# Optimization experiments

Hardware: AMD Instinct MI355X
Metric: run time of the kernel (lower is better)

The kernel has to match this reference:

```python
import jax, jax.numpy as jnp
import numpy as np

B, N, D = 8, 4096, 6          # clouds, points per cloud, coordinate dim
K = 64                        # max_num_neighbors in radius query
NS1, NS2 = 2048, 512          # fps ratios 0.5 and 0.25
R1, R2 = 0.2, 0.4             # ball-query radii
DIMS = {1: [6, 64, 64, 128], 2: [134, 128, 128, 256], 3: [262, 256, 512, 1024], 4: [1024, 512, 512]}


def setup_inputs():
    key = jax.random.key(0)
    k0, k1, k2 = jax.random.split(key, 3)
    inp = {}
    inp['synapse_cordi'] = jax.random.normal(k0, (B * N, D), jnp.float32)
    inp['batch_index'] = jnp.repeat(jnp.arange(B, dtype=jnp.int32), N)
    inp['weight'] = jax.random.uniform(k1, (B * N,), jnp.float32)
    k = k2
    for i, dims in DIMS.items():
        for j in range(len(dims) - 1):
            k, kw = jax.random.split(k)
            inp[f'w{i}_{j}'] = jax.random.normal(kw, (dims[j], dims[j + 1]), jnp.float32) * (1.0 / float(np.sqrt(dims[j])))
            inp[f'b{i}_{j}'] = jnp.zeros((dims[j + 1],), jnp.float32)
    return inp


def _mlp(x, params):
    # PyG MLP, plain_last=True; batch-norm at default (eval, running stats) is identity
    n = len(params)
    for i, (W, b) in enumerate(params):
        x = x @ W + b
        if i < n - 1:
            x = jax.nn.relu(x)
    return x


def _fps(pos, n_s):
    # farthest point sampling on one cloud [N, D] -> [n_s] indices (deterministic start at 0)
    d0 = jnp.sum((pos - pos[0]) ** 2, axis=-1)
    def step(mind, _):
        nxt = jnp.argmax(mind)
        mind = jnp.minimum(mind, jnp.sum((pos - pos[nxt]) ** 2, axis=-1))
        return mind, nxt
    _, idxs = jax.lax.scan(step, d0, None, length=n_s - 1)
    return jnp.concatenate([jnp.zeros((1,), idxs.dtype), idxs])


def _ball(pos, pos_q, r):
    # radius query: up to K nearest points within r for each query; [n_q,K] idx + validity mask
    d2 = jnp.sum((pos_q[:, None, :] - pos[None, :, :]) ** 2, axis=-1)  # [n_q, N]
    neg = jnp.where(d2 <= r * r, -d2, -jnp.inf)
    vals, nbr = jax.lax.top_k(neg, K)
    return nbr, vals > -jnp.inf


def _sa(x, pos, params, n_s, r):
    # Weight_Sample_Module: fps -> radius -> PointNetConv (gather, MLP, masked max-scatter)
    idx = jax.vmap(lambda p: _fps(p, n_s))(pos)                     # [B, n_s]
    pos_q = jnp.take_along_axis(pos, idx[..., None], axis=1)        # [B, n_s, D]
    nbr, valid = jax.vmap(lambda p, q: _ball(p, q, r))(pos, pos_q)  # [B, n_s, K]
    gather = lambda a: jax.vmap(lambda t, i: t[i])(a, nbr)          # [B, n_s, K, C]
    rel = gather(pos) - pos_q[:, :, None, :]
    feat = rel if x is None else jnp.concatenate([gather(x), rel], axis=-1)
    h = _mlp(feat, params)                                          # [B, n_s, K, C_out]
    h = jnp.where(valid[..., None], h, -jnp.inf)
    return jnp.max(h, axis=2), pos_q                                # max aggregation


def reference(synapse_cordi, batch_index, weight,
              w1_0, b1_0, w1_1, b1_1, w1_2, b1_2,
              w2_0, b2_0, w2_1, b2_1, w2_2, b2_2,
              w3_0, b3_0, w3_1, b3_1, w3_2, b3_2,
              w4_0, b4_0, w4_1, b4_1):
    pos = synapse_cordi.reshape(B, N, D)  # uniform clouds; batch_index = repeat(arange(B), N)
    p1 = [(w1_0, b1_0), (w1_1, b1_1), (w1_2, b1_2)]
    p2 = [(w2_0, b2_0), (w2_1, b2_1), (w2_2, b2_2)]
    p3 = [(w3_0, b3_0), (w3_1, b3_1), (w3_2, b3_2)]
    p4 = [(w4_0, b4_0), (w4_1, b4_1)]
    x1, pos1 = _sa(None, pos, p1, NS1, R1)   # [B, 2048, 128]
    x2, pos2 = _sa(x1, pos1, p2, NS2, R2)    # [B, 512, 256]
    h = _mlp(jnp.concatenate([x2, pos2], axis=-1), p3)  # [B, 512, 1024]
    g = jnp.max(h, axis=1)                   # global max pool -> [B, 1024]
    return _mlp(g, p4)                       # [B, 512]
```

## Files before the change

### kernel.cpp

```cpp
#include <hip/hip_runtime.h>
#include <math.h>

#define B_ 8
#define N_ 4096
#define D_ 6
#define K_ 64
#define NS1_ 2048
#define NS2_ 512

typedef float v2f __attribute__((ext_vector_type(2)));


__device__ __forceinline__ float dist2_rn(const float* __restrict__ a, const float* __restrict__ q) {
    float s = 0.f;
#pragma unroll
    for (int d = 0; d < 6; ++d) {
        float diff = __fsub_rn(a[d], q[d]);
        s = __fadd_rn(s, __fmul_rn(diff, diff));
    }
    return s;
}

__device__ __forceinline__ unsigned mapf(float x) {
    unsigned u = __float_as_uint(x);
    return (u & 0x80000000u) ? ~u : (u | 0x80000000u);
}
__device__ __forceinline__ float unmapf(unsigned u) {
    return __uint_as_float((u & 0x80000000u) ? (u & 0x7FFFFFFFu) : ~u);
}

template <int CTRL>
__device__ __forceinline__ double dppd(double k) {
    int lo = __double2loint(k), hi = __double2hiint(k);
    int nlo = __builtin_amdgcn_update_dpp(lo, lo, CTRL, 0xF, 0xF, false);
    int nhi = __builtin_amdgcn_update_dpp(hi, hi, CTRL, 0xF, 0xF, false);
    return __hiloint2double(nhi, nlo);
}


__device__ __forceinline__ void wait_flag(unsigned* f, int t) {
    if (t == 0) {
        while (__hip_atomic_load(f, __ATOMIC_RELAXED, __HIP_MEMORY_SCOPE_AGENT) == 0u)
            __builtin_amdgcn_s_sleep(32);
        __builtin_amdgcn_fence(__ATOMIC_ACQUIRE, "agent");
    }
    __syncthreads();
}


template <int NP, int NS>
__device__ __forceinline__ void fps_core(float* __restrict__ spos, int* __restrict__ sidx,
                                         double* __restrict__ part, int t) {
#pragma clang fp contract(off)
    constexpr int NT = 256;
    constexpr int P = NP / NT;
    constexpr int HP = P / 2;
    int lane = t & 63, w = t >> 6;

    v2f px2[HP][6];
#pragma unroll
    for (int j = 0; j < HP; ++j)
#pragma unroll
        for (int d = 0; d < 6; ++d) {
            px2[j][d].x = spos[(t + NT * (2 * j)) * 6 + d];
            px2[j][d].y = spos[(t + NT * (2 * j + 1)) * 6 + d];
        }

    float cx[6];
#pragma unroll
    for (int d = 0; d < 6; ++d) cx[d] = spos[d];

    v2f mind2[HP];
    float runv = -1.f;
    int runj = 0;
#pragma unroll
    for (int j = 0; j < HP; ++j) {
        v2f d2 = {0.f, 0.f};
#pragma unroll
        for (int d = 0; d < 6; ++d) {
            v2f df = px2[j][d] - cx[d];
            d2 = d2 + df * df;
        }
        mind2[j] = d2;
        if (d2.x > runv) { runv = d2.x; runj = t + NT * (2 * j); }
        if (d2.y > runv) { runv = d2.y; runj = t + NT * (2 * j + 1); }
    }

    for (int s = 1; s < NS; ++s) {
        double key = __hiloint2double((int)__float_as_uint(runv), (int)(unsigned)(~runj));
        key = fmax(key, dppd<0x111>(key));
        key = fmax(key, dppd<0x112>(key));
        key = fmax(key, dppd<0x114>(key));
        key = fmax(key, dppd<0x118>(key));
        key = fmax(key, dppd<0x142>(key));
        key = fmax(key, dppd<0x143>(key));
        if (lane == 63) part[(s & 1) * 4 + w] = key;
        __syncthreads();
        double kk = part[(s & 1) * 4 + (lane & 3)];
        kk = fmax(kk, dppd<0x111>(kk));
        kk = fmax(kk, dppd<0x112>(kk));
        int nx = ~__builtin_amdgcn_readlane(__double2loint(kk), 3);
        if (t == 0) sidx[s] = nx;

        const float2* sv2 = (const float2*)spos;
        float2 ca = sv2[nx * 3], cb = sv2[nx * 3 + 1], cc = sv2[nx * 3 + 2];
        cx[0] = ca.x; cx[1] = ca.y; cx[2] = cb.x; cx[3] = cb.y; cx[4] = cc.x; cx[5] = cc.y;

        runv = -1.f;
        runj = 0;
#pragma unroll
        for (int j = 0; j < HP; ++j) {
            v2f d2 = {0.f, 0.f};
#pragma unroll
            for (int d = 0; d < 6; ++d) {
                v2f df = px2[j][d] - cx[d];
                d2 = d2 + df * df;
            }
            float mx = fminf(mind2[j].x, d2.x);
            float my = fminf(mind2[j].y, d2.y);
            mind2[j].x = mx;
            mind2[j].y = my;
            if (mx > runv) { runv = mx; runj = t + NT * (2 * j); }
            if (my > runv) { runv = my; runj = t + NT * (2 * j + 1); }
        }
    }
}


template <int NPTS, int S>
__device__ __forceinline__ int ball_scan(const float* __restrict__ sp,
                                         const float* __restrict__ posq,
                                         float r2, int qid, int tid,
                                         float* __restrict__ sd, unsigned short* __restrict__ si) {
    float q[6];
#pragma unroll
    for (int d = 0; d < 6; ++d) q[d] = posq[(size_t)qid * 6 + d];

    int n = 0;
    float thr = INFINITY;
#pragma unroll 4
    for (int j = 0; j < NPTS; ++j) {
        float d2 = dist2_rn(sp + j * 6, q);
        if (d2 <= r2 && (n < K_ || d2 < thr)) {
            int i = (n < K_) ? n : (K_ - 1);
            if (n < K_) ++n;
            while (i > 0 && sd[(i - 1) * S + tid] > d2) {
                sd[i * S + tid] = sd[(i - 1) * S + tid];
                si[i * S + tid] = si[(i - 1) * S + tid];
                --i;
            }
            sd[i * S + tid] = d2;
            si[i * S + tid] = (unsigned short)j;
            if (n == K_) thr = sd[(K_ - 1) * S + tid];
        }
    }
    return n;
}


__global__ __launch_bounds__(256, 1) void stage12_kernel(
        const float* __restrict__ pos, float* __restrict__ pos1, float* __restrict__ pos2,
        float* __restrict__ x1, int* __restrict__ nbr2, int* __restrict__ cnt2,
        unsigned* __restrict__ g, unsigned* flags,
        const float* __restrict__ W1_0, const float* __restrict__ B1_0,
        const float* __restrict__ W1_1, const float* __restrict__ B1_1,
        const float* __restrict__ W1_2, const float* __restrict__ B1_2,
        float r2_1, float r2_2) {
    __shared__ union Smem {
        struct { float spos[N_ * 6]; int sidx[NS1_]; double part[8]; } fps;
        struct { float spos[N_ * 6]; float sd[K_ * 128]; unsigned short si[K_ * 128];
                 unsigned short scnt[128]; } p1;
        struct { float spos1[NS1_ * 6]; float sd2[K_ * 64]; unsigned short si2[K_ * 64]; } b2;
    } sm;
    int t = threadIdx.x;
    int lane = t & 63, w = t >> 6;

    if (blockIdx.x < 8) {
        int b = blockIdx.x;
        float* spos = sm.fps.spos;
        int* sidx = sm.fps.sidx;
        double* part = sm.fps.part;

        {
            const float4* src = (const float4*)(pos + (size_t)b * N_ * 6);
            float4* dst = (float4*)spos;
            for (int e = t; e < N_ * 6 / 4; e += 256) dst[e] = src[e];
        }
        if (t == 0) sidx[0] = 0;
        __syncthreads();

        fps_core<N_, NS1_>(spos, sidx, part, t);
        __syncthreads();

        float smp[NS1_ / 256][6];
#pragma unroll
        for (int i = 0; i < NS1_ / 256; ++i) {
            int s = t + 256 * i;
            int ix = sidx[s];
#pragma unroll
            for (int d = 0; d < 6; ++d) smp[i][d] = spos[ix * 6 + d];
        }
#pragma unroll
        for (int i = 0; i < NS1_ / 256; ++i) {
            int s = t + 256 * i;
#pragma unroll
            for (int d = 0; d < 6; ++d) pos1[((size_t)b * NS1_ + s) * 6 + d] = smp[i][d];
        }
        __syncthreads();
        if (t == 0) {
            __threadfence();
            __hip_atomic_store(&flags[b], 1u, __ATOMIC_RELEASE, __HIP_MEMORY_SCOPE_AGENT);
        }

#pragma unroll
        for (int i = 0; i < NS1_ / 256; ++i) {
            int s = t + 256 * i;
#pragma unroll
            for (int d = 0; d < 6; ++d) spos[s * 6 + d] = smp[i][d];
        }
        for (int e = t; e < 1024; e += 256) g[b * 1024 + e] = 0u;
        if (t == 0) sidx[0] = 0;
        __syncthreads();

        fps_core<NS1_, NS2_>(spos, sidx, part, t);
        __syncthreads();

        for (int s = t; s < NS2_; s += 256) {
            int ix = sidx[s];
#pragma unroll
            for (int d = 0; d < 6; ++d) pos2[((size_t)b * NS2_ + s) * 6 + d] = spos[ix * 6 + d];
        }
        __syncthreads();
        if (t == 0) {
            __threadfence();
            __hip_atomic_store(&flags[8 + b], 1u, __ATOMIC_RELEASE, __HIP_MEMORY_SCOPE_AGENT);
        }
    } else if (blockIdx.x < 8 + 128) {
        int blk = blockIdx.x - 8;
        int b = blk >> 4;
        {
            const float4* src = (const float4*)(pos + (size_t)b * N_ * 6);
            float4* dst = (float4*)sm.p1.spos;
            for (int e = t; e < N_ * 6 / 4; e += 256) dst[e] = src[e];
        }
        __syncthreads();
        wait_flag(&flags[b], t);

        int qbase1 = b * NS1_ + (blk & 15) * 128;
        if (t < 128) {
            int n = ball_scan<N_, 128>(sm.p1.spos, pos1, r2_1, qbase1 + t, t, sm.p1.sd, sm.p1.si);
            sm.p1.scnt[t] = (unsigned short)n;
        }
        __syncthreads();

        for (int qq = 0; qq < 32; ++qq) {
            int lq = w * 32 + qq;
            int qid = qbase1 + lq;
            float q[6];
#pragma unroll
            for (int d = 0; d < 6; ++d) q[d] = pos1[(size_t)qid * 6 + d];
            int c = sm.p1.scnt[lq];
            float m0 = -INFINITY, m1 = -INFINITY;
            for (int n = 0; n < c; ++n) {
                int j = sm.p1.si[n * 128 + lq];
                float rel[6];
#pragma unroll
                for (int d = 0; d < 6; ++d) rel[d] = sm.p1.spos[j * 6 + d] - q[d];
                float a = B1_0[lane];
#pragma unroll
                for (int d = 0; d < 6; ++d) a = fmaf(W1_0[d * 64 + lane], rel[d], a);
                float h1 = fmaxf(a, 0.f);
                float a2 = B1_1[lane];
                for (int k = 0; k < 64; ++k) {
                    float v = __shfl(h1, k, 64);
                    a2 = fmaf(W1_1[k * 64 + lane], v, a2);
                }
                float h2 = fmaxf(a2, 0.f);
                float o0 = B1_2[lane], o1 = B1_2[64 + lane];
                for (int k = 0; k < 64; ++k) {
                    float v = __shfl(h2, k, 64);
                    o0 = fmaf(W1_2[k * 128 + lane], v, o0);
                    o1 = fmaf(W1_2[k * 128 + 64 + lane], v, o1);
                }
                m0 = fmaxf(m0, o0);
                m1 = fmaxf(m1, o1);
            }
            x1[(size_t)qid * 128 + lane] = m0;
            x1[(size_t)qid * 128 + 64 + lane] = m1;
        }
    } else {
        int blk = blockIdx.x - 136;
        int b = blk >> 3;
        wait_flag(&flags[b], t);
        {
            const float4* src = (const float4*)(pos1 + (size_t)b * NS1_ * 6);
            float4* dst = (float4*)sm.b2.spos1;
            for (int e = t; e < NS1_ * 6 / 4; e += 256) dst[e] = src[e];
        }
        __syncthreads();
        wait_flag(&flags[8 + b], t);
        if (t < 64) {
            int qid = blk * 64 + t;
            int n = ball_scan<NS1_, 64>(sm.b2.spos1, pos2, r2_2, qid, t, sm.b2.sd2, sm.b2.si2);
            cnt2[qid] = n;
            for (int i = 0; i < n; ++i) nbr2[(size_t)qid * K_ + i] = (int)sm.b2.si2[i * 64 + t];
        }
    }
}


__global__ __launch_bounds__(256, 1) void sa2_mlp3_kernel(
        const float* __restrict__ pos1, const float* __restrict__ pos2,
        const int* __restrict__ nbr, const int* __restrict__ cnt,
        const float* __restrict__ x1,
        const float* __restrict__ W1, const float* __restrict__ B1,
        const float* __restrict__ W2, const float* __restrict__ B2,
        const float* __restrict__ W3, const float* __restrict__ B3,
        const float* __restrict__ M0, const float* __restrict__ MB0,
        const float* __restrict__ M1, const float* __restrict__ MB1,
        const float* __restrict__ M2, const float* __restrict__ MB2,
        unsigned* __restrict__ g) {
    __shared__ float sx2[16 * 256];
    int lane = threadIdx.x & 63;
    int w = threadIdx.x >> 6;
    int qbase = blockIdx.x * 16;
    int b = qbase >> 9;

    for (int qq = 0; qq < 4; ++qq) {
        int lq = w * 4 + qq;
        int qid = qbase + lq;
        float q[6];
#pragma unroll
        for (int d = 0; d < 6; ++d) q[d] = pos2[(size_t)qid * 6 + d];
        int c = cnt[qid];
        float m0 = -INFINITY, m1 = -INFINITY, m2 = -INFINITY, m3 = -INFINITY;
        for (int n = 0; n < c; ++n) {
            int j = nbr[(size_t)qid * K_ + n];
            size_t row = (size_t)b * NS1_ + j;
            const float* xs = x1 + row * 128;
            float rel[6];
#pragma unroll
            for (int d = 0; d < 6; ++d) rel[d] = pos1[row * 6 + d] - q[d];
            float a0e = B1[lane], a0o = 0.f, a1e = B1[64 + lane], a1o = 0.f;
            for (int k = 0; k < 128; k += 2) {
                float v0 = xs[k], v1 = xs[k + 1];
                a0e = fmaf(W1[k * 128 + lane], v0, a0e);
                a1e = fmaf(W1[k * 128 + 64 + lane], v0, a1e);
                a0o = fmaf(W1[(k + 1) * 128 + lane], v1, a0o);
                a1o = fmaf(W1[(k + 1) * 128 + 64 + lane], v1, a1o);
            }
            float a0 = a0e + a0o, a1 = a1e + a1o;
#pragma unroll
            for (int d = 0; d < 6; ++d) {
                float v = rel[d];
                a0 = fmaf(W1[(128 + d) * 128 + lane], v, a0);
                a1 = fmaf(W1[(128 + d) * 128 + 64 + lane], v, a1);
            }
            float h1a = fmaxf(a0, 0.f), h1b = fmaxf(a1, 0.f);
            float c0 = B2[lane], c1 = B2[64 + lane];
            for (int k = 0; k < 64; ++k) {
                float v = __shfl(h1a, k, 64);
                c0 = fmaf(W2[k * 128 + lane], v, c0);
                c1 = fmaf(W2[k * 128 + 64 + lane], v, c1);
            }
            for (int k = 0; k < 64; ++k) {
                float v = __shfl(h1b, k, 64);
                c0 = fmaf(W2[(64 + k) * 128 + lane], v, c0);
                c1 = fmaf(W2[(64 + k) * 128 + 64 + lane], v, c1);
            }
            float h2a = fmaxf(c0, 0.f), h2b = fmaxf(c1, 0.f);
            float e0 = B3[lane], e1 = B3[64 + lane], e2 = B3[128 + lane], e3 = B3[192 + lane];
            for (int k = 0; k < 64; ++k) {
                float v = __shfl(h2a, k, 64);
                e0 = fmaf(W3[k * 256 + lane], v, e0);
                e1 = fmaf(W3[k * 256 + 64 + lane], v, e1);
                e2 = fmaf(W3[k * 256 + 128 + lane], v, e2);
                e3 = fmaf(W3[k * 256 + 192 + lane], v, e3);
            }
            for (int k = 0; k < 64; ++k) {
                float v = __shfl(h2b, k, 64);
                e0 = fmaf(W3[(64 + k) * 256 + lane], v, e0);
                e1 = fmaf(W3[(64 + k) * 256 + 64 + lane], v, e1);
                e2 = fmaf(W3[(64 + k) * 256 + 128 + lane], v, e2);
                e3 = fmaf(W3[(64 + k) * 256 + 192 + lane], v, e3);
            }
            m0 = fmaxf(m0, e0);
            m1 = fmaxf(m1, e1);
            m2 = fmaxf(m2, e2);
            m3 = fmaxf(m3, e3);
        }
        sx2[lq * 256 + lane] = m0;
        sx2[lq * 256 + 64 + lane] = m1;
        sx2[lq * 256 + 128 + lane] = m2;
        sx2[lq * 256 + 192 + lane] = m3;
    }
    __syncthreads();

    int lq0 = w * 4;
    int qid0 = qbase + lq0;

    float xr[4][4];
#pragma unroll
    for (int q = 0; q < 4; ++q)
#pragma unroll
        for (int j = 0; j < 4; ++j) xr[q][j] = sx2[(lq0 + q) * 256 + j * 64 + lane];

    float a[4][4];
    {
        float4 bv = *(const float4*)&MB0[lane * 4];
#pragma unroll
        for (int q = 0; q < 4; ++q) { a[q][0] = bv.x; a[q][1] = bv.y; a[q][2] = bv.z; a[q][3] = bv.w; }
    }
#pragma unroll
    for (int j = 0; j < 4; ++j) {
        for (int k2 = 0; k2 < 64; ++k2) {
            int k = j * 64 + k2;
            float4 wv = *(const float4*)&M0[(size_t)k * 256 + lane * 4];
#pragma unroll
            for (int q = 0; q < 4; ++q) {
                float v = __shfl(xr[q][j], k2, 64);
                a[q][0] = fmaf(wv.x, v, a[q][0]);
                a[q][1] = fmaf(wv.y, v, a[q][1]);
                a[q][2] = fmaf(wv.z, v, a[q][2]);
                a[q][3] = fmaf(wv.w, v, a[q][3]);
            }
        }
    }
#pragma unroll
    for (int d = 0; d < 6; ++d) {
        float4 wv = *(const float4*)&M0[(size_t)(256 + d) * 256 + lane * 4];
#pragma unroll
        for (int q = 0; q < 4; ++q) {
            float v = pos2[(size_t)(qid0 + q) * 6 + d];
            a[q][0] = fmaf(wv.x, v, a[q][0]);
            a[q][1] = fmaf(wv.y, v, a[q][1]);
            a[q][2] = fmaf(wv.z, v, a[q][2]);
            a[q][3] = fmaf(wv.w, v, a[q][3]);
        }
    }
    float h1[4][4];
#pragma unroll
    for (int q = 0; q < 4; ++q)
#pragma unroll
        for (int u = 0; u < 4; ++u) h1[q][u] = fmaxf(a[q][u], 0.f);

    float c[4][8];
    {
        float4 b0 = *(const float4*)&MB1[lane * 8];
        float4 b1 = *(const float4*)&MB1[lane * 8 + 4];
#pragma unroll
        for (int q = 0; q < 4; ++q) {
            c[q][0] = b0.x; c[q][1] = b0.y; c[q][2] = b0.z; c[q][3] = b0.w;
            c[q][4] = b1.x; c[q][5] = b1.y; c[q][6] = b1.z; c[q][7] = b1.w;
        }
    }
    for (int l = 0; l < 64; ++l) {
#pragma unroll
        for (int r = 0; r < 4; ++r) {
            int k = l * 4 + r;
            float4 w0 = *(const float4*)&M1[(size_t)k * 512 + lane * 8];
            float4 w1 = *(const float4*)&M1[(size_t)k * 512 + lane * 8 + 4];
#pragma unroll
            for (int q = 0; q < 4; ++q) {
                float v = __shfl(h1[q][r], l, 64);
                c[q][0] = fmaf(w0.x, v, c[q][0]);
                c[q][1] = fmaf(w0.y, v, c[q][1]);
                c[q][2] = fmaf(w0.z, v, c[q][2]);
                c[q][3] = fmaf(w0.w, v, c[q][3]);
                c[q][4] = fmaf(w1.x, v, c[q][4]);
                c[q][5] = fmaf(w1.y, v, c[q][5]);
                c[q][6] = fmaf(w1.z, v, c[q][6]);
                c[q][7] = fmaf(w1.w, v, c[q][7]);
            }
        }
    }
    float h2[4][8];
#pragma unroll
    for (int q = 0; q < 4; ++q)
#pragma unroll
        for (int u = 0; u < 8; ++u) h2[q][u] = fmaxf(c[q][u], 0.f);

    float e[4][16];
#pragma unroll
    for (int jj = 0; jj < 4; ++jj) {
        float4 bv = *(const float4*)&MB2[lane * 16 + jj * 4];
#pragma unroll
        for (int q = 0; q < 4; ++q) {
            e[q][jj * 4 + 0] = bv.x; e[q][jj * 4 + 1] = bv.y;
            e[q][jj * 4 + 2] = bv.z; e[q][jj * 4 + 3] = bv.w;
        }
    }
    for (int l = 0; l < 64; ++l) {
#pragma unroll
        for (int r = 0; r < 8; ++r) {
            int k = l * 8 + r;
            const float* wp = &M2[(size_t)k * 1024 + lane * 16];
            float4 w0 = *(const float4*)&wp[0];
            float4 w1 = *(const float4*)&wp[4];
            float4 w2 = *(const float4*)&wp[8];
            float4 w3 = *(const float4*)&wp[12];
#pragma unroll
            for (int q = 0; q < 4; ++q) {
                float v = __shfl(h2[q][r], l, 64);
                e[q][0]  = fmaf(w0.x, v, e[q][0]);
                e[q][1]  = fmaf(w0.y, v, e[q][1]);
                e[q][2]  = fmaf(w0.z, v, e[q][2]);
                e[q][3]  = fmaf(w0.w, v, e[q][3]);
                e[q][4]  = fmaf(w1.x, v, e[q][4]);
                e[q][5]  = fmaf(w1.y, v, e[q][5]);
                e[q][6]  = fmaf(w1.z, v, e[q][6]);
                e[q][7]  = fmaf(w1.w, v, e[q][7]);
                e[q][8]  = fmaf(w2.x, v, e[q][8]);
                e[q][9]  = fmaf(w2.y, v, e[q][9]);
                e[q][10] = fmaf(w2.z, v, e[q][10]);
                e[q][11] = fmaf(w2.w, v, e[q][11]);
                e[q][12] = fmaf(w3.x, v, e[q][12]);
                e[q][13] = fmaf(w3.y, v, e[q][13]);
                e[q][14] = fmaf(w3.z, v, e[q][14]);
                e[q][15] = fmaf(w3.w, v, e[q][15]);
            }
        }
    }
#pragma unroll
    for (int u = 0; u < 16; ++u) {
        float m = fmaxf(fmaxf(e[0][u], e[1][u]), fmaxf(e[2][u], e[3][u]));
        atomicMax(&g[b * 1024 + lane * 16 + u], mapf(m));
    }
}


__global__ __launch_bounds__(512) void mlp4_kernel(const unsigned* __restrict__ g,
                                                   const float* __restrict__ W0, const float* __restrict__ B0,
                                                   const float* __restrict__ W1, const float* __restrict__ B1,
                                                   float* __restrict__ out) {
    int b = blockIdx.x;
    int c = threadIdx.x;
    __shared__ float h[512];
    float a0 = B0[c], a1 = 0.f, a2 = 0.f, a3 = 0.f;
    for (int k = 0; k < 1024; k += 4) {
        float v0 = unmapf(g[b * 1024 + k]);
        float v1 = unmapf(g[b * 1024 + k + 1]);
        float v2 = unmapf(g[b * 1024 + k + 2]);
        float v3 = unmapf(g[b * 1024 + k + 3]);
        a0 = fmaf(v0, W0[k * 512 + c], a0);
        a1 = fmaf(v1, W0[(k + 1) * 512 + c], a1);
        a2 = fmaf(v2, W0[(k + 2) * 512 + c], a2);
        a3 = fmaf(v3, W0[(k + 3) * 512 + c], a3);
    }
    h[c] = fmaxf((a0 + a1) + (a2 + a3), 0.f);
    __syncthreads();
    float o0 = B1[c], o1 = 0.f, o2 = 0.f, o3 = 0.f;
    for (int k = 0; k < 512; k += 4) {
        o0 = fmaf(h[k], W1[k * 512 + c], o0);
        o1 = fmaf(h[k + 1], W1[(k + 1) * 512 + c], o1);
        o2 = fmaf(h[k + 2], W1[(k + 2) * 512 + c], o2);
        o3 = fmaf(h[k + 3], W1[(k + 3) * 512 + c], o3);
    }
    out[(size_t)b * 512 + c] = (o0 + o1) + (o2 + o3);
}


extern "C" void kernel_launch(void* const* d_in, const int* in_sizes, int n_in,
                              void* d_out, int out_size, void* d_ws, size_t ws_size,
                              hipStream_t stream) {
    const float* pos = (const float*)d_in[0];
    const float* w1_0 = (const float*)d_in[3];
    const float* b1_0 = (const float*)d_in[4];
    const float* w1_1 = (const float*)d_in[5];
    const float* b1_1 = (const float*)d_in[6];
    const float* w1_2 = (const float*)d_in[7];
    const float* b1_2 = (const float*)d_in[8];
    const float* w2_0 = (const float*)d_in[9];
    const float* b2_0 = (const float*)d_in[10];
    const float* w2_1 = (const float*)d_in[11];
    const float* b2_1 = (const float*)d_in[12];
    const float* w2_2 = (const float*)d_in[13];
    const float* b2_2 = (const float*)d_in[14];
    const float* w3_0 = (const float*)d_in[15];
    const float* b3_0 = (const float*)d_in[16];
    const float* w3_1 = (const float*)d_in[17];
    const float* b3_1 = (const float*)d_in[18];
    const float* w3_2 = (const float*)d_in[19];
    const float* b3_2 = (const float*)d_in[20];
    const float* w4_0 = (const float*)d_in[21];
    const float* b4_0 = (const float*)d_in[22];
    const float* w4_1 = (const float*)d_in[23];
    const float* b4_1 = (const float*)d_in[24];
    float* out = (float*)d_out;

    char* ws = (char*)d_ws;
    size_t off = 0;
    float* pos1 = (float*)(ws + off);    off += (size_t)B_ * NS1_ * 6 * 4;
    float* pos2 = (float*)(ws + off);    off += (size_t)B_ * NS2_ * 6 * 4;
    float* x1 = (float*)(ws + off);      off += (size_t)B_ * NS1_ * 128 * 4;
    int* nbr2 = (int*)(ws + off);        off += (size_t)B_ * NS2_ * K_ * 4;
    int* cnt2 = (int*)(ws + off);        off += (size_t)B_ * NS2_ * 4;
    unsigned* g = (unsigned*)(ws + off); off += (size_t)B_ * 1024 * 4;
    unsigned* flags = (unsigned*)(ws + off); off += 16 * 4;

    const float r2_1 = (float)(0.2 * 0.2);
    const float r2_2 = (float)(0.4 * 0.4);

    hipMemsetAsync(flags, 0, 16 * 4, stream);

    stage12_kernel<<<200, 256, 0, stream>>>(pos, pos1, pos2, x1, nbr2, cnt2, g, flags,
                                            w1_0, b1_0, w1_1, b1_1, w1_2, b1_2,
                                            r2_1, r2_2);
    sa2_mlp3_kernel<<<(B_ * NS2_) / 16, 256, 0, stream>>>(pos1, pos2, nbr2, cnt2, x1,
                                                          w2_0, b2_0, w2_1, b2_1, w2_2, b2_2,
                                                          w3_0, b3_0, w3_1, b3_1, w3_2, b3_2, g);
    mlp4_kernel<<<B_, 512, 0, stream>>>(g, w4_0, b4_0, w4_1, b4_1, out);
}
```

Baseline: 2.498 ms.

## Fuse final MLP into tail kernel via last-block-per-batch atomic counter

Removes the separate mlp4 kernel launch. Each block of the SA2+MLP3 kernel increments a per-batch done counter after its atomicMax into the global pool, and the last of the 32 blocks for that batch runs the two-layer head MLP. This saves a kernel launch and its gap. The cost is that the head MLP now runs on only 256 threads with non-unrolled serial accumulation, inside a kernel sized for one block per CU. The flags buffer is enlarged to hold the counters.

```diff
diff --git a/kernel.cpp b/kernel.cpp
--- a/kernel.cpp
+++ b/kernel.cpp
@@ -309,7 +309,7 @@
 }
 
 
-__global__ __launch_bounds__(256, 1) void sa2_mlp3_kernel(
+__global__ __launch_bounds__(256, 1) void tail_kernel(
         const float* __restrict__ pos1, const float* __restrict__ pos2,
         const int* __restrict__ nbr, const int* __restrict__ cnt,
         const float* __restrict__ x1,
@@ -319,10 +319,15 @@
         const float* __restrict__ M0, const float* __restrict__ MB0,
         const float* __restrict__ M1, const float* __restrict__ MB1,
         const float* __restrict__ M2, const float* __restrict__ MB2,
-        unsigned* __restrict__ g) {
+        const float* __restrict__ W4_0, const float* __restrict__ B4_0,
+        const float* __restrict__ W4_1, const float* __restrict__ B4_1,
+        unsigned* __restrict__ g, unsigned* done, float* __restrict__ out) {
     __shared__ float sx2[16 * 256];
-    int lane = threadIdx.x & 63;
-    int w = threadIdx.x >> 6;
+    __shared__ float h4[512];
+    __shared__ unsigned slast;
+    int t = threadIdx.x;
+    int lane = t & 63;
+    int w = t >> 6;
     int qbase = blockIdx.x * 16;
     int b = qbase >> 9;
 
@@ -396,167 +401,165 @@
     }
     __syncthreads();
 
-    int lq0 = w * 4;
-    int qid0 = qbase + lq0;
-
-    float xr[4][4];
-#pragma unroll
-    for (int q = 0; q < 4; ++q)
-#pragma unroll
-        for (int j = 0; j < 4; ++j) xr[q][j] = sx2[(lq0 + q) * 256 + j * 64 + lane];
-
-    float a[4][4];
     {
-        float4 bv = *(const float4*)&MB0[lane * 4];
-#pragma unroll
-        for (int q = 0; q < 4; ++q) { a[q][0] = bv.x; a[q][1] = bv.y; a[q][2] = bv.z; a[q][3] = bv.w; }
-    }
-#pragma unroll
-    for (int j = 0; j < 4; ++j) {
-        for (int k2 = 0; k2 < 64; ++k2) {
-            int k = j * 64 + k2;
-            float4 wv = *(const float4*)&M0[(size_t)k * 256 + lane * 4];
+        int lq0 = w * 4;
+        int qid0 = qbase + lq0;
+
+        float xr[4][4];
+#pragma unroll
+        for (int q = 0; q < 4; ++q)
+#pragma unroll
+            for (int j = 0; j < 4; ++j) xr[q][j] = sx2[(lq0 + q) * 256 + j * 64 + lane];
+
+        float a[4][4];
+        {
+            float4 bv = *(const float4*)&MB0[lane * 4];
+#pragma unroll
+            for (int q = 0; q < 4; ++q) { a[q][0] = bv.x; a[q][1] = bv.y; a[q][2] = bv.z; a[q][3] = bv.w; }
+        }
+#pragma unroll
+        for (int j = 0; j < 4; ++j) {
+            for (int k2 = 0; k2 < 64; ++k2) {
+                int k = j * 64 + k2;
+                float4 wv = *(const float4*)&M0[(size_t)k * 256 + lane * 4];
+#pragma unroll
+                for (int q = 0; q < 4; ++q) {
+                    float v = __shfl(xr[q][j], k2, 64);
+                    a[q][0] = fmaf(wv.x, v, a[q][0]);
+                    a[q][1] = fmaf(wv.y, v, a[q][1]);
+                    a[q][2] = fmaf(wv.z, v, a[q][2]);
+                    a[q][3] = fmaf(wv.w, v, a[q][3]);
+                }
+            }
+        }
+#pragma unroll
+        for (int d = 0; d < 6; ++d) {
+            float4 wv = *(const float4*)&M0[(size_t)(256 + d) * 256 + lane * 4];
 #pragma unroll
             for (int q = 0; q < 4; ++q) {
-                float v = __shfl(xr[q][j], k2, 64);
+                float v = pos2[(size_t)(qid0 + q) * 6 + d];
                 a[q][0] = fmaf(wv.x, v, a[q][0]);
                 a[q][1] = fmaf(wv.y, v, a[q][1]);
                 a[q][2] = fmaf(wv.z, v, a[q][2]);
                 a[q][3] = fmaf(wv.w, v, a[q][3]);
             }
         }
-    }
-#pragma unroll
-    for (int d = 0; d < 6; ++d) {
-        float4 wv = *(const float4*)&M0[(size_t)(256 + d) * 256 + lane * 4];
-#pragma unroll
-        for (int q = 0; q < 4; ++q) {
-            float v = pos2[(size_t)(qid0 + q) * 6 + d];
-            a[q][0] = fmaf(wv.x, v, a[q][0]);
-            a[q][1] = fmaf(wv.y, v, a[q][1]);
-            a[q][2] = fmaf(wv.z, v, a[q][2]);
-            a[q][3] = fmaf(wv.w, v, a[q][3]);
-        }
-    }
-    float h1[4][4];
-#pragma unroll
-    for (int q = 0; q < 4; ++q)
-#pragma unroll
-        for (int u = 0; u < 4; ++u) h1[q][u] = fmaxf(a[q][u], 0.f);
-
-    float c[4][8];
-    {
-        float4 b0 = *(const float4*)&MB1[lane * 8];
-        float4 b1 = *(const float4*)&MB1[lane * 8 + 4];
-#pragma unroll
-        for (int q = 0; q < 4; ++q) {
-            c[q][0] = b0.x; c[q][1] = b0.y; c[q][2] = b0.z; c[q][3] = b0.w;
-            c[q][4] = b1.x; c[q][5] = b1.y; c[q][6] = b1.z; c[q][7] = b1.w;
-        }
-    }
-    for (int l = 0; l < 64; ++l) {
-#pragma unroll
-        for (int r = 0; r < 4; ++r) {
-            int k = l * 4 + r;
-            float4 w0 = *(const float4*)&M1[(size_t)k * 512 + lane * 8];
-            float4 w1 = *(const float4*)&M1[(size_t)k * 512 + lane * 8 + 4];
+        float h1[4][4];
+#pragma unroll
+        for (int q = 0; q < 4; ++q)
+#pragma unroll
+            for (int u = 0; u < 4; ++u) h1[q][u] = fmaxf(a[q][u], 0.f);
+
+        float c[4][8];
+        {
+            float4 b0 = *(const float4*)&MB1[lane * 8];
+            float4 b1 = *(const float4*)&MB1[lane * 8 + 4];
 #pragma unroll
             for (int q = 0; q < 4; ++q) {
-                float v = __shfl(h1[q][r], l, 64);
-                c[q][0] = fmaf(w0.x, v, c[q][0]);
-                c[q][1] = fmaf(w0.y, v, c[q][1]);
-                c[q][2] = fmaf(w0.z, v, c[q][2]);
-                c[q][3] = fmaf(w0.w, v, c[q][3]);
-                c[q][4] = fmaf(w1.x, v, c[q][4]);
-                c[q][5] = fmaf(w1.y, v, c[q][5]);
-                c[q][6] = fmaf(w1.z, v, c[q][6]);
-                c[q][7] = fmaf(w1.w, v, c[q][7]);
-            }
-        }
-    }
-    float h2[4][8];
-#pragma unroll
-    for (int q = 0; q < 4; ++q)
-#pragma unroll
-        for (int u = 0; u < 8; ++u) h2[q][u] = fmaxf(c[q][u], 0.f);
-
-    float e[4][16];
-#pragma unroll
-    for (int jj = 0; jj < 4; ++jj) {
-        float4 bv = *(const float4*)&MB2[lane * 16 + jj * 4];
-#pragma unroll
-        for (int q = 0; q < 4; ++q) {
-            e[q][jj * 4 + 0] = bv.x; e[q][jj * 4 + 1] = bv.y;
-            e[q][jj * 4 + 2] = bv.z; e[q][jj * 4 + 3] = bv.w;
-        }
-    }
-    for (int l = 0; l < 64; ++l) {
-#pragma unroll
-        for (int r = 0; r < 8; ++r) {
-            int k = l * 8 + r;
-            const float* wp = &M2[(size_t)k * 1024 + lane * 16];
-            float4 w0 = *(const float4*)&wp[0];
-            float4 w1 = *(const float4*)&wp[4];
-            float4 w2 = *(const float4*)&wp[8];
-            float4 w3 = *(const float4*)&wp[12];
+                c[q][0] = b0.x; c[q][1] = b0.y; c[q][2] = b0.z; c[q][3] = b0.w;
+                c[q][4] = b1.x; c[q][5] = b1.y; c[q][6] = b1.z; c[q][7] = b1.w;
+            }
+        }
+        for (int l = 0; l < 64; ++l) {
+#pragma unroll
+            for (int r = 0; r < 4; ++r) {
+                int k = l * 4 + r;
+                float4 w0 = *(const float4*)&M1[(size_t)k * 512 + lane * 8];
+                float4 w1 = *(const float4*)&M1[(size_t)k * 512 + lane * 8 + 4];
+#pragma unroll
+                for (int q = 0; q < 4; ++q) {
+                    float v = __shfl(h1[q][r], l, 64);
+                    c[q][0] = fmaf(w0.x, v, c[q][0]);
+                    c[q][1] = fmaf(w0.y, v, c[q][1]);
+                    c[q][2] = fmaf(w0.z, v, c[q][2]);
+                    c[q][3] = fmaf(w0.w, v, c[q][3]);
+                    c[q][4] = fmaf(w1.x, v, c[q][4]);
+                    c[q][5] = fmaf(w1.y, v, c[q][5]);
+                    c[q][6] = fmaf(w1.z, v, c[q][6]);
+                    c[q][7] = fmaf(w1.w, v, c[q][7]);
+                }
+            }
+        }
+        float h2[4][8];
+#pragma unroll
+        for (int q = 0; q < 4; ++q)
+#pragma unroll
+            for (int u = 0; u < 8; ++u) h2[q][u] = fmaxf(c[q][u], 0.f);
+
+        float e[4][16];
+#pragma unroll
+        for (int jj = 0; jj < 4; ++jj) {
+            float4 bv = *(const float4*)&MB2[lane * 16 + jj * 4];
 #pragma unroll
             for (int q = 0; q < 4; ++q) {
-                float v = __shfl(h2[q][r], l, 64);
-                e[q][0]  = fmaf(w0.x, v, e[q][0]);
-                e[q][1]  = fmaf(w0.y, v, e[q][1]);
-                e[q][2]  = fmaf(w0.z, v, e[q][2]);
-                e[q][3]  = fmaf(w0.w, v, e[q][3]);
-                e[q][4]  = fmaf(w1.x, v, e[q][4]);
-                e[q][5]  = fmaf(w1.y, v, e[q][5]);
-                e[q][6]  = fmaf(w1.z, v, e[q][6]);
-                e[q][7]  = fmaf(w1.w, v, e[q][7]);
-                e[q][8]  = fmaf(w2.x, v, e[q][8]);
-                e[q][9]  = fmaf(w2.y, v, e[q][9]);
-                e[q][10] = fmaf(w2.z, v, e[q][10]);
-                e[q][11] = fmaf(w2.w, v, e[q][11]);
-                e[q][12] = fmaf(w3.x, v, e[q][12]);
-                e[q][13] = fmaf(w3.y, v, e[q][13]);
-                e[q][14] = fmaf(w3.z, v, e[q][14]);
-                e[q][15] = fmaf(w3.w, v, e[q][15]);
-            }
-        }
-    }
-#pragma unroll
-    for (int u = 0; u < 16; ++u) {
-        float m = fmaxf(fmaxf(e[0][u], e[1][u]), fmaxf(e[2][u], e[3][u]));
-        atomicMax(&g[b * 1024 + lane * 16 + u], mapf(m));
-    }
-}
-
-
-__global__ __launch_bounds__(512) void mlp4_kernel(const unsigned* __restrict__ g,
-                                                   const float* __restrict__ W0, const float* __restrict__ B0,
-                                                   const float* __restrict__ W1, const float* __restrict__ B1,
-                                                   float* __restrict__ out) {
-    int b = blockIdx.x;
-    int c = threadIdx.x;
-    __shared__ float h[512];
-    float a0 = B0[c], a1 = 0.f, a2 = 0.f, a3 = 0.f;
-    for (int k = 0; k < 1024; k += 4) {
-        float v0 = unmapf(g[b * 1024 + k]);
-        float v1 = unmapf(g[b * 1024 + k + 1]);
-        float v2 = unmapf(g[b * 1024 + k + 2]);
-        float v3 = unmapf(g[b * 1024 + k + 3]);
-        a0 = fmaf(v0, W0[k * 512 + c], a0);
-        a1 = fmaf(v1, W0[(k + 1) * 512 + c], a1);
-        a2 = fmaf(v2, W0[(k + 2) * 512 + c], a2);
-        a3 = fmaf(v3, W0[(k + 3) * 512 + c], a3);
-    }
-    h[c] = fmaxf((a0 + a1) + (a2 + a3), 0.f);
+                e[q][jj * 4 + 0] = bv.x; e[q][jj * 4 + 1] = bv.y;
+                e[q][jj * 4 + 2] = bv.z; e[q][jj * 4 + 3] = bv.w;
+            }
+        }
+        for (int l = 0; l < 64; ++l) {
+#pragma unroll
+            for (int r = 0; r < 8; ++r) {
+                int k = l * 8 + r;
+                const float* wp = &M2[(size_t)k * 1024 + lane * 16];
+                float4 w0 = *(const float4*)&wp[0];
+                float4 w1 = *(const float4*)&wp[4];
+                float4 w2 = *(const float4*)&wp[8];
+                float4 w3 = *(const float4*)&wp[12];
+#pragma unroll
+                for (int q = 0; q < 4; ++q) {
+                    float v = __shfl(h2[q][r], l, 64);
+                    e[q][0]  = fmaf(w0.x, v, e[q][0]);
+                    e[q][1]  = fmaf(w0.y, v, e[q][1]);
+                    e[q][2]  = fmaf(w0.z, v, e[q][2]);
+                    e[q][3]  = fmaf(w0.w, v, e[q][3]);
+                    e[q][4]  = fmaf(w1.x, v, e[q][4]);
+                    e[q][5]  = fmaf(w1.y, v, e[q][5]);
+                    e[q][6]  = fmaf(w1.z, v, e[q][6]);
+                    e[q][7]  = fmaf(w1.w, v, e[q][7]);
+                    e[q][8]  = fmaf(w2.x, v, e[q][8]);
+                    e[q][9]  = fmaf(w2.y, v, e[q][9]);
+                    e[q][10] = fmaf(w2.z, v, e[q][10]);
+                    e[q][11] = fmaf(w2.w, v, e[q][11]);
+                    e[q][12] = fmaf(w3.x, v, e[q][12]);
+                    e[q][13] = fmaf(w3.y, v, e[q][13]);
+                    e[q][14] = fmaf(w3.z, v, e[q][14]);
+                    e[q][15] = fmaf(w3.w, v, e[q][15]);
+                }
+            }
+        }
+#pragma unroll
+        for (int u = 0; u < 16; ++u) {
+            float m = fmaxf(fmaxf(e[0][u], e[1][u]), fmaxf(e[2][u], e[3][u]));
+            atomicMax(&g[b * 1024 + lane * 16 + u], mapf(m));
+        }
+    }
+
     __syncthreads();
-    float o0 = B1[c], o1 = 0.f, o2 = 0.f, o3 = 0.f;
-    for (int k = 0; k < 512; k += 4) {
-        o0 = fmaf(h[k], W1[k * 512 + c], o0);
-        o1 = fmaf(h[k + 1], W1[(k + 1) * 512 + c], o1);
-        o2 = fmaf(h[k + 2], W1[(k + 2) * 512 + c], o2);
-        o3 = fmaf(h[k + 3], W1[(k + 3) * 512 + c], o3);
-    }
-    out[(size_t)b * 512 + c] = (o0 + o1) + (o2 + o3);
+    if (t == 0) {
+        __threadfence();
+        unsigned old = __hip_atomic_fetch_add(&done[b], 1u, __ATOMIC_ACQ_REL,
+                                              __HIP_MEMORY_SCOPE_AGENT);
+        slast = (old == 31u) ? 1u : 0u;
+    }
+    __syncthreads();
+    if (slast) {
+        if (t == 0) __builtin_amdgcn_fence(__ATOMIC_ACQUIRE, "agent");
+        __syncthreads();
+        for (int ch = t; ch < 512; ch += 256) {
+            float a = B4_0[ch];
+            for (int k = 0; k < 1024; ++k) {
+                float v = unmapf(g[b * 1024 + k]);
+                a = fmaf(v, W4_0[k * 512 + ch], a);
+            }
+            h4[ch] = fmaxf(a, 0.f);
+        }
+        __syncthreads();
+        for (int ch = t; ch < 512; ch += 256) {
+            float o = B4_1[ch];
+            for (int k = 0; k < 512; ++k) o = fmaf(h4[k], W4_1[k * 512 + ch], o);
+            out[(size_t)b * 512 + ch] = o;
+        }
+    }
 }
 
 
@@ -596,18 +599,19 @@
     int* nbr2 = (int*)(ws + off);        off += (size_t)B_ * NS2_ * K_ * 4;
     int* cnt2 = (int*)(ws + off);        off += (size_t)B_ * NS2_ * 4;
     unsigned* g = (unsigned*)(ws + off); off += (size_t)B_ * 1024 * 4;
-    unsigned* flags = (unsigned*)(ws + off); off += 16 * 4;
+    unsigned* flags = (unsigned*)(ws + off); off += 64 * 4;
 
     const float r2_1 = (float)(0.2 * 0.2);
     const float r2_2 = (float)(0.4 * 0.4);
 
-    hipMemsetAsync(flags, 0, 16 * 4, stream);
+    hipMemsetAsync(flags, 0, 64 * 4, stream);
 
     stage12_kernel<<<200, 256, 0, stream>>>(pos, pos1, pos2, x1, nbr2, cnt2, g, flags,
                                             w1_0, b1_0, w1_1, b1_1, w1_2, b1_2,
                                             r2_1, r2_2);
-    sa2_mlp3_kernel<<<(B_ * NS2_) / 16, 256, 0, stream>>>(pos1, pos2, nbr2, cnt2, x1,
-                                                          w2_0, b2_0, w2_1, b2_1, w2_2, b2_2,
-                                                          w3_0, b3_0, w3_1, b3_1, w3_2, b3_2, g);
-    mlp4_kernel<<<B_, 512, 0, stream>>>(g, w4_0, b4_0, w4_1, b4_1, out);
-}
+    tail_kernel<<<(B_ * NS2_) / 16, 256, 0, stream>>>(pos1, pos2, nbr2, cnt2, x1,
+                                                      w2_0, b2_0, w2_1, b2_1, w2_2, b2_2,
+                                                      w3_0, b3_0, w3_1, b3_1, w3_2, b3_2,
+                                                      w4_0, b4_0, w4_1, b4_1,
+                                                      g, flags + 40, out);
+}
```

Measured after the change: 2.635 ms. 1.05x slower.

## Double stage12 block size to 512 threads and pack MLP3 FMAs into v2f

Applied to the files above, without the earlier changes.

Launches the stage12 kernel with 512 threads per block, so the serial FPS loop spreads the point set over 8 waves with a deeper cross-wave argmax reduction, and ball-query blocks each take half as many queries per wave. Separately, the MLP3 accumulators in sa2_mlp3_kernel are rewritten as two-wide float vectors so the compiler can emit packed FMA instructions. The wider FPS block aims to shorten the per-step latency of the sequential sampling, at the cost of a larger reduction and possibly more register pressure under the 512-thread launch bound. Some ball-query loops that still assume 256 threads are not visible, so correctness there is uncertain.

```diff
diff --git a/kernel.cpp b/kernel.cpp
--- a/kernel.cpp
+++ b/kernel.cpp
@@ -48,11 +48,11 @@
 }
 
 
-template <int NP, int NS>
+template <int NP, int NS, int NT>
 __device__ __forceinline__ void fps_core(float* __restrict__ spos, int* __restrict__ sidx,
                                          double* __restrict__ part, int t) {
 #pragma clang fp contract(off)
-    constexpr int NT = 256;
+    constexpr int NW = NT / 64;
     constexpr int P = NP / NT;
     constexpr int HP = P / 2;
     int lane = t & 63, w = t >> 6;
@@ -94,12 +94,13 @@
         key = fmax(key, dppd<0x118>(key));
         key = fmax(key, dppd<0x142>(key));
         key = fmax(key, dppd<0x143>(key));
-        if (lane == 63) part[(s & 1) * 4 + w] = key;
-        __syncthreads();
-        double kk = part[(s & 1) * 4 + (lane & 3)];
+        if (lane == 63) part[(s & 1) * NW + w] = key;
+        __syncthreads();
+        double kk = part[(s & 1) * NW + (lane & (NW - 1))];
         kk = fmax(kk, dppd<0x111>(kk));
         kk = fmax(kk, dppd<0x112>(kk));
-        int nx = ~__builtin_amdgcn_readlane(__double2loint(kk), 3);
+        if constexpr (NW == 8) kk = fmax(kk, dppd<0x114>(kk));
+        int nx = ~__builtin_amdgcn_readlane(__double2loint(kk), NW - 1);
         if (t == 0) sidx[s] = nx;
 
         const float2* sv2 = (const float2*)spos;
@@ -158,7 +159,7 @@
 }
 
 
-__global__ __launch_bounds__(256, 1) void stage12_kernel(
+__global__ __launch_bounds__(512, 1) void stage12_kernel(
         const float* __restrict__ pos, float* __restrict__ pos1, float* __restrict__ pos2,
         float* __restrict__ x1, int* __restrict__ nbr2, int* __restrict__ cnt2,
         unsigned* __restrict__ g, unsigned* flags,
@@ -167,7 +168,7 @@
         const float* __restrict__ W1_2, const float* __restrict__ B1_2,
         float r2_1, float r2_2) {
     __shared__ union Smem {
-        struct { float spos[N_ * 6]; int sidx[NS1_]; double part[8]; } fps;
+        struct { float spos[N_ * 6]; int sidx[NS1_]; double part[16]; } fps;
         struct { float spos[N_ * 6]; float sd[K_ * 128]; unsigned short si[K_ * 128];
                  unsigned short scnt[128]; } p1;
         struct { float spos1[NS1_ * 6]; float sd2[K_ * 64]; unsigned short si2[K_ * 64]; } b2;
@@ -184,25 +185,25 @@
         {
             const float4* src = (const float4*)(pos + (size_t)b * N_ * 6);
             float4* dst = (float4*)spos;
-            for (int e = t; e < N_ * 6 / 4; e += 256) dst[e] = src[e];
+            for (int e = t; e < N_ * 6 / 4; e += 512) dst[e] = src[e];
         }
         if (t == 0) sidx[0] = 0;
         __syncthreads();
 
-        fps_core<N_, NS1_>(spos, sidx, part, t);
-        __syncthreads();
-
-        float smp[NS1_ / 256][6];
-#pragma unroll
-        for (int i = 0; i < NS1_ / 256; ++i) {
-            int s = t + 256 * i;
+        fps_core<N_, NS1_, 512>(spos, sidx, part, t);
+        __syncthreads();
+
+        float smp[NS1_ / 512][6];
+#pragma unroll
+        for (int i = 0; i < NS1_ / 512; ++i) {
+            int s = t + 512 * i;
             int ix = sidx[s];
 #pragma unroll
             for (int d = 0; d < 6; ++d) smp[i][d] = spos[ix * 6 + d];
         }
 #pragma unroll
-        for (int i = 0; i < NS1_ / 256; ++i) {
-            int s = t + 256 * i;
+        for (int i = 0; i < NS1_ / 512; ++i) {
+            int s = t + 512 * i;
 #pragma unroll
             for (int d = 0; d < 6; ++d) pos1[((size_t)b * NS1_ + s) * 6 + d] = smp[i][d];
         }
@@ -213,19 +214,19 @@
         }
 
 #pragma unroll
-        for (int i = 0; i < NS1_ / 256; ++i) {
-            int s = t + 256 * i;
+        for (int i = 0; i < NS1_ / 512; ++i) {
+            int s = t + 512 * i;
 #pragma unroll
             for (int d = 0; d < 6; ++d) spos[s * 6 + d] = smp[i][d];
         }
-        for (int e = t; e < 1024; e += 256) g[b * 1024 + e] = 0u;
+        for (int e = t; e < 1024; e += 512) g[b * 1024 + e] = 0u;
         if (t == 0) sidx[0] = 0;
         __syncthreads();
 
-        fps_core<NS1_, NS2_>(spos, sidx, part, t);
-        __syncthreads();
-
-        for (int s = t; s < NS2_; s += 256) {
+        fps_core<NS1_, NS2_, 512>(spos, sidx, part, t);
+        __syncthreads();
+
+        for (int s = t; s < NS2_; s += 512) {
             int ix = sidx[s];
 #pragma unroll
             for (int d = 0; d < 6; ++d) pos2[((size_t)b * NS2_ + s) * 6 + d] = spos[ix * 6 + d];
@@ -241,7 +242,7 @@
         {
             const float4* src = (const float4*)(pos + (size_t)b * N_ * 6);
             float4* dst = (float4*)sm.p1.spos;
-            for (int e = t; e < N_ * 6 / 4; e += 256) dst[e] = src[e];
+            for (int e = t; e < N_ * 6 / 4; e += 512) dst[e] = src[e];
         }
         __syncthreads();
         wait_flag(&flags[b], t);
@@ -253,8 +254,8 @@
         }
         __syncthreads();
 
-        for (int qq = 0; qq < 32; ++qq) {
-            int lq = w * 32 + qq;
+        for (int qq = 0; qq < 16; ++qq) {
+            int lq = w * 16 + qq;
             int qid = qbase1 + lq;
             float q[6];
 #pragma unroll
@@ -295,7 +296,7 @@
         {
             const float4* src = (const float4*)(pos1 + (size_t)b * NS1_ * 6);
             float4* dst = (float4*)sm.b2.spos1;
-            for (int e = t; e < NS1_ * 6 / 4; e += 256) dst[e] = src[e];
+            for (int e = t; e < NS1_ * 6 / 4; e += 512) dst[e] = src[e];
         }
         __syncthreads();
         wait_flag(&flags[8 + b], t);
@@ -405,54 +406,56 @@
 #pragma unroll
         for (int j = 0; j < 4; ++j) xr[q][j] = sx2[(lq0 + q) * 256 + j * 64 + lane];
 
-    float a[4][4];
+    v2f a[4][2];
     {
         float4 bv = *(const float4*)&MB0[lane * 4];
-#pragma unroll
-        for (int q = 0; q < 4; ++q) { a[q][0] = bv.x; a[q][1] = bv.y; a[q][2] = bv.z; a[q][3] = bv.w; }
+        v2f b0 = {bv.x, bv.y}, b1 = {bv.z, bv.w};
+#pragma unroll
+        for (int q = 0; q < 4; ++q) { a[q][0] = b0; a[q][1] = b1; }
     }
 #pragma unroll
     for (int j = 0; j < 4; ++j) {
         for (int k2 = 0; k2 < 64; ++k2) {
             int k = j * 64 + k2;
             float4 wv = *(const float4*)&M0[(size_t)k * 256 + lane * 4];
+            v2f w0 = {wv.x, wv.y}, w1 = {wv.z, wv.w};
 #pragma unroll
             for (int q = 0; q < 4; ++q) {
                 float v = __shfl(xr[q][j], k2, 64);
-                a[q][0] = fmaf(wv.x, v, a[q][0]);
-                a[q][1] = fmaf(wv.y, v, a[q][1]);
-                a[q][2] = fmaf(wv.z, v, a[q][2]);
-                a[q][3] = fmaf(wv.w, v, a[q][3]);
+                v2f vv = {v, v};
+                a[q][0] = __builtin_elementwise_fma(w0, vv, a[q][0]);
+                a[q][1] = __builtin_elementwise_fma(w1, vv, a[q][1]);
             }
         }
     }
 #pragma unroll
     for (int d = 0; d < 6; ++d) {
         float4 wv = *(const float4*)&M0[(size_t)(256 + d) * 256 + lane * 4];
+        v2f w0 = {wv.x, wv.y}, w1 = {wv.z, wv.w};
 #pragma unroll
         for (int q = 0; q < 4; ++q) {
             float v = pos2[(size_t)(qid0 + q) * 6 + d];
-            a[q][0] = fmaf(wv.x, v, a[q][0]);
-            a[q][1] = fmaf(wv.y, v, a[q][1]);
-            a[q][2] = fmaf(wv.z, v, a[q][2]);
-            a[q][3] = fmaf(wv.w, v, a[q][3]);
+            v2f vv = {v, v};
+            a[q][0] = __builtin_elementwise_fma(w0, vv, a[q][0]);
+            a[q][1] = __builtin_elementwise_fma(w1, vv, a[q][1]);
         }
     }
     float h1[4][4];
 #pragma unroll
-    for (int q = 0; q < 4; ++q)
-#pragma unroll
-        for (int u = 0; u < 4; ++u) h1[q][u] = fmaxf(a[q][u], 0.f);
-
-    float c[4][8];
+    for (int q = 0; q < 4; ++q) {
+        h1[q][0] = fmaxf(a[q][0].x, 0.f);
+        h1[q][1] = fmaxf(a[q][0].y, 0.f);
+        h1[q][2] = fmaxf(a[q][1].x, 0.f);
+        h1[q][3] = fmaxf(a[q][1].y, 0.f);
+    }
+
+    v2f c[4][4];
     {
         float4 b0 = *(const float4*)&MB1[lane * 8];
         float4 b1 = *(const float4*)&MB1[lane * 8 + 4];
-#pragma unroll
-        for (int q = 0; q < 4; ++q) {
-            c[q][0] = b0.x; c[q][1] = b0.y; c[q][2] = b0.z; c[q][3] = b0.w;
-            c[q][4] = b1.x; c[q][5] = b1.y; c[q][6] = b1.z; c[q][7] = b1.w;
-        }
+        v2f p0 = {b0.x, b0.y}, p1 = {b0.z, b0.w}, p2 = {b1.x, b1.y}, p3 = {b1.z, b1.w};
+#pragma unroll
+        for (int q = 0; q < 4; ++q) { c[q][0] = p0; c[q][1] = p1; c[q][2] = p2; c[q][3] = p3; }
     }
     for (int l = 0; l < 64; ++l) {
 #pragma unroll
@@ -460,17 +463,15 @@
             int k = l * 4 + r;
             float4 w0 = *(const float4*)&M1[(size_t)k * 512 + lane * 8];
             float4 w1 = *(const float4*)&M1[(size_t)k * 512 + lane * 8 + 4];
+            v2f p0 = {w0.x, w0.y}, p1 = {w0.z, w0.w}, p2 = {w1.x, w1.y}, p3 = {w1.z, w1.w};
 #pragma unroll
             for (int q = 0; q < 4; ++q) {
                 float v = __shfl(h1[q][r], l, 64);
-                c[q][0] = fmaf(w0.x, v, c[q][0]);
-                c[q][1] = fmaf(w0.y, v, c[q][1]);
-                c[q][2] = fmaf(w0.z, v, c[q][2]);
-                c[q][3] = fmaf(w0.w, v, c[q][3]);
-                c[q][4] = fmaf(w1.x, v, c[q][4]);
-                c[q][5] = fmaf(w1.y, v, c[q][5]);
-                c[q][6] = fmaf(w1.z, v, c[q][6]);
-                c[q][7] = fmaf(w1.w, v, c[q][7]);
+                v2f vv = {v, v};
+                c[q][0] = __builtin_elementwise_fma(p0, vv, c[q][0]);
+                c[q][1] = __builtin_elementwise_fma(p1, vv, c[q][1]);
+                c[q][2] = __builtin_elementwise_fma(p2, vv, c[q][2]);
+                c[q][3] = __builtin_elementwise_fma(p3, vv, c[q][3]);
             }
         }
     }
@@ -478,17 +479,18 @@
 #pragma unroll
     for (int q = 0; q < 4; ++q)
 #pragma unroll
-        for (int u = 0; u < 8; ++u) h2[q][u] = fmaxf(c[q][u], 0.f);
-
-    float e[4][16];
+        for (int p = 0; p < 4; ++p) {
+            h2[q][2 * p] = fmaxf(c[q][p].x, 0.f);
+            h2[q][2 * p + 1] = fmaxf(c[q][p].y, 0.f);
+        }
+
+    v2f e[4][8];
 #pragma unroll
     for (int jj = 0; jj < 4; ++jj) {
         float4 bv = *(const float4*)&MB2[lane * 16 + jj * 4];
-#pragma unroll
-        for (int q = 0; q < 4; ++q) {
-            e[q][jj * 4 + 0] = bv.x; e[q][jj * 4 + 1] = bv.y;
-            e[q][jj * 4 + 2] = bv.z; e[q][jj * 4 + 3] = bv.w;
-        }
+        v2f p0 = {bv.x, bv.y}, p1 = {bv.z, bv.w};
+#pragma unroll
+        for (int q = 0; q < 4; ++q) { e[q][jj * 2] = p0; e[q][jj * 2 + 1] = p1; }
     }
     for (int l = 0; l < 64; ++l) {
 #pragma unroll
@@ -499,32 +501,29 @@
             float4 w1 = *(const float4*)&wp[4];
             float4 w2 = *(const float4*)&wp[8];
             float4 w3 = *(const float4*)&wp[12];
+            v2f p0 = {w0.x, w0.y}, p1 = {w0.z, w0.w}, p2 = {w1.x, w1.y}, p3 = {w1.z, w1.w};
+            v2f p4 = {w2.x, w2.y}, p5 = {w2.z, w2.w}, p6 = {w3.x, w3.y}, p7 = {w3.z, w3.w};
 #pragma unroll
             for (int q = 0; q < 4; ++q) {
                 float v = __shfl(h2[q][r], l, 64);
-                e[q][0]  = fmaf(w0.x, v, e[q][0]);
-                e[q][1]  = fmaf(w0.y, v, e[q][1]);
-                e[q][2]  = fmaf(w0.z, v, e[q][2]);
-                e[q][3]  = fmaf(w0.w, v, e[q][3]);
-                e[q][4]  = fmaf(w1.x, v, e[q][4]);
-                e[q][5]  = fmaf(w1.y, v, e[q][5]);
-                e[q][6]  = fmaf(w1.z, v, e[q][6]);
-                e[q][7]  = fmaf(w1.w, v, e[q][7]);
-                e[q][8]  = fmaf(w2.x, v, e[q][8]);
-                e[q][9]  = fmaf(w2.y, v, e[q][9]);
-                e[q][10] = fmaf(w2.z, v, e[q][10]);
-                e[q][11] = fmaf(w2.w, v, e[q][11]);
-                e[q][12] = fmaf(w3.x, v, e[q][12]);
-                e[q][13] = fmaf(w3.y, v, e[q][13]);
-                e[q][14] = fmaf(w3.z, v, e[q][14]);
-                e[q][15] = fmaf(w3.w, v, e[q][15]);
-            }
-        }
-    }
-#pragma unroll
-    for (int u = 0; u < 16; ++u) {
-        float m = fmaxf(fmaxf(e[0][u], e[1][u]), fmaxf(e[2][u], e[3][u]));
-        atomicMax(&g[b * 1024 + lane * 16 + u], mapf(m));
+                v2f vv = {v, v};
+                e[q][0] = __builtin_elementwise_fma(p0, vv, e[q][0]);
+                e[q][1] = __builtin_elementwise_fma(p1, vv, e[q][1]);
+                e[q][2] = __builtin_elementwise_fma(p2, vv, e[q][2]);
+                e[q][3] = __builtin_elementwise_fma(p3, vv, e[q][3]);
+                e[q][4] = __builtin_elementwise_fma(p4, vv, e[q][4]);
+                e[q][5] = __builtin_elementwise_fma(p5, vv, e[q][5]);
+                e[q][6] = __builtin_elementwise_fma(p6, vv, e[q][6]);
+                e[q][7] = __builtin_elementwise_fma(p7, vv, e[q][7]);
+            }
+        }
+    }
+#pragma unroll
+    for (int p = 0; p < 8; ++p) {
+        float mx = fmaxf(fmaxf(e[0][p].x, e[1][p].x), fmaxf(e[2][p].x, e[3][p].x));
+        float my = fmaxf(fmaxf(e[0][p].y, e[1][p].y), fmaxf(e[2][p].y, e[3][p].y));
+        atomicMax(&g[b * 1024 + lane * 16 + 2 * p], mapf(mx));
+        atomicMax(&g[b * 1024 + lane * 16 + 2 * p + 1], mapf(my));
     }
 }
 
@@ -603,7 +602,7 @@
 
     hipMemsetAsync(flags, 0, 16 * 4, stream);
 
-    stage12_kernel<<<200, 256, 0, stream>>>(pos, pos1, pos2, x1, nbr2, cnt2, g, flags,
+    stage12_kernel<<<200, 512, 0, stream>>>(pos, pos1, pos2, x1, nbr2, cnt2, g, flags,
                                             w1_0, b1_0, w1_1, b1_1, w1_2, b1_2,
                                             r2_1, r2_2);
     sa2_mlp3_kernel<<<(B_ * NS2_) / 16, 256, 0, stream>>>(pos1, pos2, nbr2, cnt2, x1,
```

Result: no change. 2.537 ms (+1.5%).
